# Kernel optimization log

Hardware: AMD Instinct MI355X
Metric: run time of the kernel (lower is better)

The kernel has to match this reference:

```python
import jax, jax.numpy as jnp
import numpy as np
from jax import lax

# 4th-order Butterworth lowpass, scipy.signal.butter(4, 0.2)
B_COEF = np.array([0.004824343357716228, 0.019297373430864913, 0.02894606014629737,
                   0.019297373430864913, 0.004824343357716228], dtype=np.float32)
A_COEF = np.array([1.0, -2.369513007182038, 2.3139884144006453,
                   -1.0546654058785672, 0.18737949236818502], dtype=np.float32)


def setup_inputs() -> dict:
    key = jax.random.key(0)
    x = jax.random.normal(key, (8, 64, 48000), dtype=jnp.float32)
    return {"x": x, "b": jnp.asarray(B_COEF), "a": jnp.asarray(A_COEF)}


def _pad_odd(x, n):
    # Faithful to torch _pad_odd (including its exact slicing on the right side).
    left = 2.0 * x[..., 0:1] - jnp.flip(x[..., 0:n], axis=-1)
    right = 2.0 * x[..., -1:] - jnp.flip(x[..., -(n + 2):-2], axis=-1)
    return jnp.concatenate([left, x, right], axis=-1)


def _lfilter(x, a, b):
    # y[n] = (sum_k b[k] x[n-k] - sum_j a[j] y[n-j]) / a[0]
    a0 = a[0]
    bn = b / a0
    an = a[1:] / a0                      # [N], N = order
    ntaps = b.shape[0]                   # static
    N = a.shape[0] - 1                   # static
    T = x.shape[-1]
    # FIR part: small static tap loop, fully vectorized over batch/time.
    pad = [(0, 0)] * (x.ndim - 1) + [(ntaps - 1, 0)]
    xp = jnp.pad(x, pad)
    f = bn[0] * xp[..., ntaps - 1: ntaps - 1 + T]
    for k in range(1, ntaps):
        f = f + bn[k] * xp[..., ntaps - 1 - k: ntaps - 1 - k + T]
    # IIR recurrence via scan over time.
    f_t = jnp.moveaxis(f, -1, 0)         # [T, B, C]
    init = jnp.zeros(x.shape[:-1] + (N,), x.dtype)  # [B, C, N], y[t-1..t-N]

    def step(carry, ft):
        y = ft - jnp.einsum('k,...k->...', an, carry)
        carry = jnp.concatenate([y[..., None], carry[..., :-1]], axis=-1)
        return carry, y

    _, ys = lax.scan(step, init, f_t)
    return jnp.moveaxis(ys, 0, -1)       # [B, C, T]


def _filtfilt(x, a, b):
    y = _lfilter(x, a, b)
    return jnp.flip(_lfilter(jnp.flip(y, axis=-1), a, b), axis=-1)


def reference(x, b, a):
    scale = jnp.max(jnp.abs(x), axis=-1, keepdims=True)
    xs = x / scale
    padlen = 3 * max(int(a.shape[0]), int(b.shape[0]))  # 15, static
    xp = _pad_odd(xs, padlen)
    y = _filtfilt(xp, a, b)
    y = y[..., padlen:-padlen]
    return y * scale
```

## Files before the change

### kernel.cpp

```cpp
#include <hip/hip_runtime.h>


#define T48 48000
#define TP0 48030
#define LCH 24
#define UPB 504

#define BAR_LDS() do { \
  asm volatile("s_waitcnt lgkmcnt(0)" ::: "memory"); \
  __builtin_amdgcn_s_barrier(); \
} while (0)

__device__ __forceinline__ float fget(const float4& v, int e) {
  switch (e & 3) { case 0: return v.x; case 1: return v.y; case 2: return v.z; default: return v.w; }
}

#define MAPPLY(t, M, q) do { \
  (t).x += (M)[0]*(q).x  + (M)[1]*(q).y  + (M)[2]*(q).z  + (M)[3]*(q).w; \
  (t).y += (M)[4]*(q).x  + (M)[5]*(q).y  + (M)[6]*(q).z  + (M)[7]*(q).w; \
  (t).z += (M)[8]*(q).x  + (M)[9]*(q).y  + (M)[10]*(q).z + (M)[11]*(q).w; \
  (t).w += (M)[12]*(q).x + (M)[13]*(q).y + (M)[14]*(q).z + (M)[15]*(q).w; \
} while (0)

struct Cf { float b0,b1,b2,b3,b4, na1,na2,na3,na4; };

template<bool PRE>
__device__ __forceinline__ void pass_pipeline(
    const int t, const int gc, const float4* __restrict__ F,
    const float* __restrict__ xs, float4* __restrict__ os4,
    const float (* __restrict__ P)[16], float4* __restrict__ S, const Cf cf,
    const float4* __restrict__ xn4, const int fbn, float4* __restrict__ FB)
{
  const float b0 = cf.b0, b1 = cf.b1, b2 = cf.b2, b3 = cf.b3, b4 = cf.b4;
  const float na1 = cf.na1, na2 = cf.na2, na3 = cf.na3, na4 = cf.na4;

  float w4v = F[0].y, w3v = F[0].z, w2v = F[0].w, w1v = F[1].x;
  float A[LCH];
#pragma unroll
  for (int n = 0; n < LCH; n++) A[n] = fget(F[(n + 5) >> 2], (n + 5) & 3);

  if (gc < 0) {
    w4v = 0.f; w3v = 0.f; w2v = 0.f; w1v = 0.f;
#pragma unroll
    for (int n = 0; n < LCH; n++) A[n] = 0.f;
  } else if (gc == 0) {
    float x0d = 2.f * xs[0];
    w4v = 0.f; w3v = 0.f; w2v = 0.f; w1v = 0.f;
#pragma unroll
    for (int n = 0; n < 15; n++) A[n] = x0d - xs[14 - n];
  }
  if (gc >= 2000) {
    float xld = 2.f * xs[T48 - 1];
#define RFIX(p, var) do { int _p = (p); \
    if (_p >= 48015) var = (_p < TP0) ? (xld - xs[96012 - _p]) : 0.f; } while (0)
    RFIX(24*gc - 4, w4v); RFIX(24*gc - 3, w3v);
    RFIX(24*gc - 2, w2v); RFIX(24*gc - 1, w1v);
#pragma unroll
    for (int n = 0; n < LCH; n++) {
      int p = 24*gc + n;
      if (p >= 48015) A[n] = (p < TP0) ? (xld - xs[96012 - p]) : 0.f;
    }
#undef RFIX
  }

  if constexpr (PRE) {
#pragma unroll
    for (int k = 0; k < 4; k++) {
      int m = min(max(fbn + k, 0), 11999);
      FB[k] = xn4[m];
    }
  }

  float r1 = 0.f, r2 = 0.f, r3 = 0.f, r4 = 0.f;
#pragma unroll
  for (int n = 0; n < LCH; n++) {
    float xv = A[n];
    float f = fmaf(b0,xv, fmaf(b1,w1v, fmaf(b2,w2v, fmaf(b3,w3v, b4*w4v))));
    w4v = w3v; w3v = w2v; w2v = w1v; w1v = xv;
    float u = fmaf(na4, r4, f);
    u = fmaf(na3, r3, u); u = fmaf(na2, r2, u); u = fmaf(na1, r1, u);
    A[n] = u; r4 = r3; r3 = r2; r2 = r1; r1 = u;
  }

  S[t] = make_float4(r1, r2, r3, r4);
  BAR_LDS();
  float4 sv = make_float4(0.f,0.f,0.f,0.f);
  if (t >= 1) sv = S[t-1];
  if (t >= 2) { float4 q = S[t-2]; MAPPLY(sv, P[0], q); }
  if (t >= 3) { float4 q = S[t-3]; MAPPLY(sv, P[1], q); }
  if (t >= 4) { float4 q = S[t-4]; MAPPLY(sv, P[2], q); }

  {
    float h1 = sv.x, h2 = sv.y, h3 = sv.z, h4 = sv.w;
#pragma unroll
    for (int n = 0; n < LCH; n++) {
      float h = fmaf(na1, h1, fmaf(na2, h2, fmaf(na3, h3, na4 * h4)));
      A[n] += h;
      h4 = h3; h3 = h2; h2 = h1; h1 = h;
    }
  }
  if (gc >= 2000) {
#pragma unroll
    for (int n = 0; n < LCH; n++) if (24*gc + n >= TP0) A[n] = 0.f;
  }

  S[512 + t] = make_float4(A[0], A[1], A[2], A[3]);
  BAR_LDS();
  float h0 = 0.f, h1v = 0.f, h2v = 0.f, h3v = 0.f;
  if (t < 511) { float4 hv = S[512 + t + 1]; h0 = hv.x; h1v = hv.y; h2v = hv.z; h3v = hv.w; }

#define YV(i) ((i) < 24 ? A[(i)] : ((i)==24 ? h0 : (i)==25 ? h1v : (i)==26 ? h2v : h3v))
  r1 = 0.f; r2 = 0.f; r3 = 0.f; r4 = 0.f;
#pragma unroll
  for (int m = 0; m < LCH; m++) {
    float g = fmaf(b0, YV(23-m), fmaf(b1, YV(24-m),
              fmaf(b2, YV(25-m), fmaf(b3, YV(26-m), b4 * YV(27-m)))));
    float u = fmaf(na4, r4, g);
    u = fmaf(na3, r3, u); u = fmaf(na2, r2, u); u = fmaf(na1, r1, u);
    r4 = r3; r3 = r2; r2 = r1; r1 = u;
    if      (m == 0) h3v = u;
    else if (m == 1) h2v = u;
    else if (m == 2) h1v = u;
    else if (m == 3) h0  = u;
    else             A[27 - m] = u;
  }
#undef YV

  if constexpr (PRE) {
#pragma unroll
    for (int k = 4; k < 8; k++) {
      int m = min(max(fbn + k, 0), 11999);
      FB[k] = xn4[m];
    }
  }

  S[1024 + t] = make_float4(r1, r2, r3, r4);
  BAR_LDS();
  float4 ev = make_float4(0.f,0.f,0.f,0.f);
  if (t <= 510) ev = S[1024 + t + 1];
  if (t <= 509) { float4 q = S[1024 + t + 2]; MAPPLY(ev, P[0], q); }
  if (t <= 508) { float4 q = S[1024 + t + 3]; MAPPLY(ev, P[1], q); }
  if (t <= 507) { float4 q = S[1024 + t + 4]; MAPPLY(ev, P[2], q); }
  BAR_LDS();

  {
    float g1 = ev.x, g2 = ev.y, g3 = ev.z, g4 = ev.w;
#pragma unroll
    for (int m = 0; m < LCH; m++) {
      float h = fmaf(na1, g1, fmaf(na2, g2, fmaf(na3, g3, na4 * g4)));
      if      (m == 0) h3v += h;
      else if (m == 1) h2v += h;
      else if (m == 2) h1v += h;
      else if (m == 3) h0  += h;
      else             A[27 - m] += h;
      g4 = g3; g3 = g2; g2 = g1; g1 = h;
    }
  }

  S[t]        = make_float4(A[4],  A[5],  A[6],  A[7]);
  S[512 + t]  = make_float4(A[8],  A[9],  A[10], A[11]);
  S[1024 + t] = make_float4(A[12], A[13], A[14], A[15]);
  S[1536 + t] = make_float4(A[16], A[17], A[18], A[19]);
  BAR_LDS();
  if (t >= 4 && t < 508 && gc <= 1999) {
    float4 N0 = S[t+1], N1 = S[512 + t+1], N2 = S[1024 + t+1], N3 = S[1536 + t+1];
    float4* op = os4 + 6*gc;
    op[0] = make_float4(A[19], A[20], A[21], A[22]);
    op[1] = make_float4(A[23], h0,    h1v,   h2v);
    op[2] = make_float4(h3v,   N0.x,  N0.y,  N0.z);
    op[3] = make_float4(N0.w,  N1.x,  N1.y,  N1.z);
    op[4] = make_float4(N1.w,  N2.x,  N2.y,  N2.z);
    op[5] = make_float4(N2.w,  N3.x,  N3.y,  N3.z);
  }
}

__global__ __launch_bounds__(512, 4) void filtfilt_k(
    const float* __restrict__ x, const float* __restrict__ bco,
    const float* __restrict__ aco, float* __restrict__ out)
{
  __shared__ __align__(16) float4 S[2048];
  __shared__ float P[3][16];

  const int t    = threadIdx.x;
  const int pair = blockIdx.x >> 2;
  const int b    = blockIdx.x & 3;
  const int gc   = UPB*b - 4 + t;
  const float* __restrict__ xsA = x + (size_t)(2*pair)     * T48;
  const float* __restrict__ xsB = x + (size_t)(2*pair + 1) * T48;
  const float4* __restrict__ xsA4 = reinterpret_cast<const float4*>(xsA);
  const float4* __restrict__ xsB4 = reinterpret_cast<const float4*>(xsB);
  float4* __restrict__ osA4 = reinterpret_cast<float4*>(out + (size_t)(2*pair)     * T48);
  float4* __restrict__ osB4 = reinterpret_cast<float4*>(out + (size_t)(2*pair + 1) * T48);

  const float inva0 = 1.f / aco[0];
  const Cf cf = { bco[0]*inva0, bco[1]*inva0, bco[2]*inva0, bco[3]*inva0, bco[4]*inva0,
                  -aco[1]*inva0, -aco[2]*inva0, -aco[3]*inva0, -aco[4]*inva0 };

  float4 FA[8];
  const int fb = 6*gc - 5;
#pragma unroll
  for (int k = 0; k < 8; k++) {
    int m = min(max(fb + k, 0), 11999);
    FA[k] = xsA4[m];
  }

  if (t < 64) {
    const int i = (t >> 2) & 3, j = t & 3;
    float r1 = (j==0)?1.f:0.f, r2 = (j==1)?1.f:0.f,
          r3 = (j==2)?1.f:0.f, r4 = (j==3)?1.f:0.f;
#pragma unroll
    for (int n = 0; n < LCH; n++) {
      float h = fmaf(cf.na1, r1, fmaf(cf.na2, r2, fmaf(cf.na3, r3, cf.na4 * r4)));
      r4 = r3; r3 = r2; r2 = r1; r1 = h;
    }
    float c0 = __shfl(r1, j), c1 = __shfl(r2, j),
          c2 = __shfl(r3, j), c3 = __shfl(r4, j);
    float Pv = (i==0)?c0 : (i==1)?c1 : (i==2)?c2 : c3;
    if (t < 16) P[0][t] = Pv;
    const float P0v = Pv;
    {
      float rA0 = __shfl(Pv, i*4+0), rA1 = __shfl(Pv, i*4+1),
            rA2 = __shfl(Pv, i*4+2), rA3 = __shfl(Pv, i*4+3);
      float cB0 = __shfl(Pv, 0*4+j), cB1 = __shfl(Pv, 1*4+j),
            cB2 = __shfl(Pv, 2*4+j), cB3 = __shfl(Pv, 3*4+j);
      Pv = rA0*cB0 + rA1*cB1 + rA2*cB2 + rA3*cB3;
    }
    if (t < 16) P[1][t] = Pv;
    {
      float rA0 = __shfl(Pv, i*4+0), rA1 = __shfl(Pv, i*4+1),
            rA2 = __shfl(Pv, i*4+2), rA3 = __shfl(Pv, i*4+3);
      float cB0 = __shfl(P0v, 0*4+j), cB1 = __shfl(P0v, 1*4+j),
            cB2 = __shfl(P0v, 2*4+j), cB3 = __shfl(P0v, 3*4+j);
      Pv = rA0*cB0 + rA1*cB1 + rA2*cB2 + rA3*cB3;
    }
    if (t < 16) P[2][t] = Pv;
  }

  float4 FB[8];
  pass_pipeline<true >(t, gc, FA, xsA, osA4, P, S, cf, xsB4, fb, FB);

  BAR_LDS();

  pass_pipeline<false>(t, gc, FB, xsB, osB4, P, S, cf, xsB4, fb, FB);
}

extern "C" void kernel_launch(void* const* d_in, const int* in_sizes, int n_in,
                              void* d_out, int out_size, void* d_ws, size_t ws_size,
                              hipStream_t stream) {
  (void)n_in; (void)d_ws; (void)ws_size; (void)out_size;
  const float* x = (const float*)d_in[0];
  const float* b = (const float*)d_in[1];
  const float* a = (const float*)d_in[2];
  float* out = (float*)d_out;
  const int nseq = in_sizes[0] / T48;
  filtfilt_k<<<dim3((nseq / 2) * 4), dim3(512), 0, stream>>>(x, b, a, out);
}
```

Before: 205.3 us.

## Process four sequences per block with chained prefetch across two pairs

```diff
diff --git a/kernel.cpp b/kernel.cpp
--- a/kernel.cpp
+++ b/kernel.cpp
@@ -24,12 +24,12 @@
 
 struct Cf { float b0,b1,b2,b3,b4, na1,na2,na3,na4; };
 
-template<bool PRE>
 __device__ __forceinline__ void pass_pipeline(
     const int t, const int gc, const float4* __restrict__ F,
     const float* __restrict__ xs, float4* __restrict__ os4,
     const float (* __restrict__ P)[16], float4* __restrict__ S, const Cf cf,
-    const float4* __restrict__ xn4, const int fbn, float4* __restrict__ FB)
+    const float4* __restrict__ xn4, const int fbn, float4* __restrict__ FB,
+    const bool pre)
 {
   const float b0 = cf.b0, b1 = cf.b1, b2 = cf.b2, b3 = cf.b3, b4 = cf.b4;
   const float na1 = cf.na1, na2 = cf.na2, na3 = cf.na3, na4 = cf.na4;
@@ -63,7 +63,7 @@
 #undef RFIX
   }
 
-  if constexpr (PRE) {
+  if (pre) {
 #pragma unroll
     for (int k = 0; k < 4; k++) {
       int m = min(max(fbn + k, 0), 11999);
@@ -126,7 +126,7 @@
   }
 #undef YV
 
-  if constexpr (PRE) {
+  if (pre) {
 #pragma unroll
     for (int k = 4; k < 8; k++) {
       int m = min(max(fbn + k, 0), 11999);
@@ -182,26 +182,25 @@
   __shared__ float P[3][16];
 
   const int t    = threadIdx.x;
-  const int pair = blockIdx.x >> 2;
+  const int quad = blockIdx.x >> 2;
   const int b    = blockIdx.x & 3;
   const int gc   = UPB*b - 4 + t;
-  const float* __restrict__ xsA = x + (size_t)(2*pair)     * T48;
-  const float* __restrict__ xsB = x + (size_t)(2*pair + 1) * T48;
-  const float4* __restrict__ xsA4 = reinterpret_cast<const float4*>(xsA);
-  const float4* __restrict__ xsB4 = reinterpret_cast<const float4*>(xsB);
-  float4* __restrict__ osA4 = reinterpret_cast<float4*>(out + (size_t)(2*pair)     * T48);
-  float4* __restrict__ osB4 = reinterpret_cast<float4*>(out + (size_t)(2*pair + 1) * T48);
 
   const float inva0 = 1.f / aco[0];
   const Cf cf = { bco[0]*inva0, bco[1]*inva0, bco[2]*inva0, bco[3]*inva0, bco[4]*inva0,
                   -aco[1]*inva0, -aco[2]*inva0, -aco[3]*inva0, -aco[4]*inva0 };
 
+  const int fb = 6*gc - 5;
+  const size_t sbase = (size_t)(4*quad) * T48;
+
   float4 FA[8];
-  const int fb = 6*gc - 5;
-#pragma unroll
-  for (int k = 0; k < 8; k++) {
-    int m = min(max(fb + k, 0), 11999);
-    FA[k] = xsA4[m];
+  {
+    const float4* __restrict__ x0 = reinterpret_cast<const float4*>(x + sbase);
+#pragma unroll
+    for (int k = 0; k < 8; k++) {
+      int m = min(max(fb + k, 0), 11999);
+      FA[k] = x0[m];
+    }
   }
 
   if (t < 64) {
@@ -237,11 +236,20 @@
   }
 
   float4 FB[8];
-  pass_pipeline<true >(t, gc, FA, xsA, osA4, P, S, cf, xsB4, fb, FB);
-
-  BAR_LDS();
-
-  pass_pipeline<false>(t, gc, FB, xsB, osB4, P, S, cf, xsB4, fb, FB);
+  for (int q = 0; q < 4; q += 2) {
+    const float* xsA = x + sbase + (size_t)q * T48;
+    const float* xsB = xsA + T48;
+    const float4* xsB4 = reinterpret_cast<const float4*>(xsB);
+    const float4* xsC4 = reinterpret_cast<const float4*>(
+        (q + 2 < 4) ? (xsB + T48) : xsB);
+    float4* osA4 = reinterpret_cast<float4*>(out + sbase + (size_t)q * T48);
+    float4* osB4 = reinterpret_cast<float4*>(out + sbase + (size_t)(q + 1) * T48);
+
+    pass_pipeline(t, gc, FA, xsA, osA4, P, S, cf, xsB4, fb, FB, true);
+    BAR_LDS();
+    pass_pipeline(t, gc, FB, xsB, osB4, P, S, cf, xsC4, fb, FA, q + 2 < 4);
+    if (q + 2 < 4) BAR_LDS();
+  }
 }
 
 extern "C" void kernel_launch(void* const* d_in, const int* in_sizes, int n_in,
@@ -253,5 +261,5 @@
   const float* a = (const float*)d_in[2];
   float* out = (float*)d_out;
   const int nseq = in_sizes[0] / T48;
-  filtfilt_k<<<dim3((nseq / 2) * 4), dim3(512), 0, stream>>>(x, b, a, out);
-}
+  filtfilt_k<<<dim3(nseq), dim3(512), 0, stream>>>(x, b, a, out);
+}
```

Measured after the change: 238.1 us. +16.0%, slower.
